# Optimization experiments

Hardware: AMD Instinct MI355X
Metric: run time of the kernel (lower is better)

The kernel has to match this reference:

```python
import jax, jax.numpy as jnp
import numpy as np

N_NODES = 50000
N_EDGES = 600000
D = 128
HIDDEN = 128
N_GRAPHS = 128
N_CLASSES = 10
N_STACKED = 3  # num_layers - 1


def setup_inputs() -> dict:
    key = jax.random.key(0)
    ks = jax.random.split(key, 12)
    s = 1.0 / np.sqrt(HIDDEN)
    inp = {
        "x": jax.random.normal(ks[0], (N_NODES, D), dtype=jnp.float32),
        "edge_index": jax.random.randint(ks[1], (2, N_EDGES), 0, N_NODES, dtype=jnp.int64),
        "batch": jnp.sort(jax.random.randint(ks[2], (N_NODES,), 0, N_GRAPHS, dtype=jnp.int64)),
        "W1": jax.random.normal(ks[3], (D, HIDDEN), dtype=jnp.float32) * s,
        "R1": jax.random.normal(ks[4], (D, HIDDEN), dtype=jnp.float32) * s,
        "b1": jnp.zeros((HIDDEN,), dtype=jnp.float32),
        "Wc": jax.random.normal(ks[5], (N_STACKED, HIDDEN, HIDDEN), dtype=jnp.float32) * s,
        "Rc": jax.random.normal(ks[6], (N_STACKED, HIDDEN, HIDDEN), dtype=jnp.float32) * s,
        "bc": jnp.zeros((N_STACKED, HIDDEN), dtype=jnp.float32),
        "lin1_w": jax.random.normal(ks[7], (HIDDEN, HIDDEN), dtype=jnp.float32) * s,
        "lin1_b": jnp.zeros((HIDDEN,), dtype=jnp.float32),
        "lin2_w": jax.random.normal(ks[8], (HIDDEN, N_CLASSES), dtype=jnp.float32) * s,
        "lin2_b": jnp.zeros((N_CLASSES,), dtype=jnp.float32),
    }
    return inp


def _gcn_norm(edge_index, n_nodes):
    # symmetric GCN normalization coeffs per edge (edge_weight=None -> ones)
    src, dst = edge_index[0], edge_index[1]
    ones = jnp.ones((edge_index.shape[1],), dtype=jnp.float32)
    deg = jax.ops.segment_sum(ones, dst, num_segments=n_nodes)
    dinv = jnp.where(deg > 0, jax.lax.rsqrt(jnp.maximum(deg, 1.0)), 0.0)
    return dinv[src] * dinv[dst]


def _gcs(x, src, dst, norm, W, R, b):
    # GCN aggregation on transformed features + linear skip (root) connection
    h = x @ W                                   # [N, H]
    msg = h[src] * norm[:, None]                # gather + scale, [E, H]
    agg = jax.ops.segment_sum(msg, dst, num_segments=x.shape[0])
    return agg + x @ R + b


def reference(x, edge_index, batch, W1, R1, b1, Wc, Rc, bc,
              lin1_w, lin1_b, lin2_w, lin2_b):
    src, dst = edge_index[0], edge_index[1]
    norm = _gcn_norm(edge_index, x.shape[0])

    h = jax.nn.relu(_gcs(x, src, dst, norm, W1, R1, b1))
    for i in range(N_STACKED):
        h = jax.nn.relu(_gcs(h, src, dst, norm, Wc[i], Rc[i], bc[i]))
    last = h

    # global mean pool over graphs
    sums = jax.ops.segment_sum(h, batch, num_segments=N_GRAPHS)
    cnts = jax.ops.segment_sum(jnp.ones((h.shape[0],), h.dtype), batch,
                               num_segments=N_GRAPHS)
    pooled = sums / jnp.maximum(cnts, 1.0)[:, None]

    g = jax.nn.relu(pooled @ lin1_w + lin1_b)   # dropout is identity in eval mode
    logits = g @ lin2_w + lin2_b
    return jax.nn.log_softmax(logits, axis=-1), last
```

## Files before the change

### kernel.cpp

```cpp
#include <hip/hip_runtime.h>

#define N_NODES  50000
#define N_EDGES  600000
#define DIM      128
#define N_GRAPHS 128
#define N_CLASSES 10
#define NB_SCAN  196
#define LDSW     136
#define NZB      6266


typedef __bf16 bf16x8 __attribute__((ext_vector_type(8)));
typedef float  f32x4  __attribute__((ext_vector_type(4)));

__device__ inline unsigned short f2bf(float f) {
  union { float f; unsigned int i; } u; u.f = f;
  unsigned int r = u.i + 0x7fff + ((u.i >> 16) & 1);
  return (unsigned short)(r >> 16);
}
__device__ inline float bf2f(unsigned short s) {
  union { unsigned int i; float f; } u; u.i = ((unsigned int)s) << 16;
  return u.f;
}
__device__ inline bf16x8 pack8(float4 lo, float4 hi) {
  union { bf16x8 v; unsigned short s[8]; } u;
  u.s[0] = f2bf(lo.x); u.s[1] = f2bf(lo.y); u.s[2] = f2bf(lo.z); u.s[3] = f2bf(lo.w);
  u.s[4] = f2bf(hi.x); u.s[5] = f2bf(hi.y); u.s[6] = f2bf(hi.z); u.s[7] = f2bf(hi.w);
  return u.v;
}


__global__ __launch_bounds__(256) void k_prep(float* __restrict__ zbase,
                                              const float* __restrict__ W1,
                                              const float* __restrict__ R1,
                                              const float* __restrict__ Wc,
                                              const float* __restrict__ Rc,
                                              unsigned short* __restrict__ pk) {
  if (blockIdx.x < NZB) {
    int i = blockIdx.x * 256 + threadIdx.x;
    if (i < 1604000) zbase[i] = 0.f;
    return;
  }
  int pb = blockIdx.x - NZB;
  int mm = pb >> 3, sub = pb & 7;
  const float* src = (mm == 0) ? W1
                   : (mm < 4)  ? Wc + (size_t)(mm - 1) * DIM * DIM
                   : (mm == 4) ? R1
                               : Rc + (size_t)(mm - 5) * DIM * DIM;
  int idx = sub * 256 + threadIdx.x;
  int lane = idx & 63;
  int kc   = (idx >> 6) & 3;
  int nt   = idx >> 8;
  int col  = nt * 16 + (lane & 15);
  int k0   = kc * 32 + (lane >> 4) * 8;
  unsigned short* dst = pk + (size_t)mm * 16384 + (size_t)idx * 8;
  ushort4 u;
  u.x = f2bf(src[(k0 + 0) * DIM + col]);
  u.y = f2bf(src[(k0 + 1) * DIM + col]);
  u.z = f2bf(src[(k0 + 2) * DIM + col]);
  u.w = f2bf(src[(k0 + 3) * DIM + col]);
  *(ushort4*)&dst[0] = u;
  u.x = f2bf(src[(k0 + 4) * DIM + col]);
  u.y = f2bf(src[(k0 + 5) * DIM + col]);
  u.z = f2bf(src[(k0 + 6) * DIM + col]);
  u.w = f2bf(src[(k0 + 7) * DIM + col]);
  *(ushort4*)&dst[4] = u;
}


__global__ __launch_bounds__(256) void k_deg(const int* __restrict__ ei,
                                             int* __restrict__ deg) {
  int e = blockIdx.x * 256 + threadIdx.x;
  if (e < N_EDGES) atomicAdd(&deg[ei[N_EDGES + e]], 1);
}

__global__ __launch_bounds__(256) void k_dinvsum(const int* __restrict__ deg,
                                                 float* __restrict__ dinv,
                                                 int* __restrict__ bsum) {
  int i = blockIdx.x * 256 + threadIdx.x;
  int t = threadIdx.x;
  int d = (i < N_NODES) ? deg[i] : 0;
  if (i < N_NODES) dinv[i] = (d > 0) ? rsqrtf((float)d) : 0.f;
  int dp = (d + 3) & ~3;
  __shared__ int tmp[256];
  tmp[t] = dp;
  __syncthreads();
  for (int off = 128; off > 0; off >>= 1) {
    if (t < off) tmp[t] += tmp[t + off];
    __syncthreads();
  }
  if (t == 0) bsum[blockIdx.x] = tmp[0];
}

__global__ __launch_bounds__(256) void k_bscan(const int* __restrict__ bsum,
                                               int* __restrict__ boff,
                                               int* __restrict__ rowp) {
  int t = threadIdx.x;
  int v = (t < NB_SCAN) ? bsum[t] : 0;
  __shared__ int tmp[256];
  tmp[t] = v;
  __syncthreads();
  for (int off = 1; off < 256; off <<= 1) {
    int add = (t >= off) ? tmp[t - off] : 0;
    __syncthreads();
    tmp[t] += add;
    __syncthreads();
  }
  boff[t] = tmp[t] - v;
  if (t == 255) rowp[N_NODES] = tmp[255];
}

__global__ __launch_bounds__(256) void k_rowp(const int* __restrict__ deg,
                                              const int* __restrict__ boff,
                                              int* __restrict__ rowp) {
  int i = blockIdx.x * 256 + threadIdx.x;
  int t = threadIdx.x;
  int dp = (i < N_NODES) ? ((deg[i] + 3) & ~3) : 0;
  __shared__ int tmp[256];
  tmp[t] = dp;
  __syncthreads();
  for (int off = 1; off < 256; off <<= 1) {
    int add = (t >= off) ? tmp[t - off] : 0;
    __syncthreads();
    tmp[t] += add;
    __syncthreads();
  }
  if (i < N_NODES) rowp[i] = boff[blockIdx.x] + tmp[t] - dp;
}

__global__ __launch_bounds__(256) void k_fill(const int* __restrict__ ei,
                                              const int* __restrict__ rowp,
                                              int* __restrict__ cnt,
                                              const float* __restrict__ dinv,
                                              int* __restrict__ csrc,
                                              float* __restrict__ enorm) {
  int e = blockIdx.x * 256 + threadIdx.x;
  if (e < N_EDGES) {
    int s = ei[e];
    int d = ei[N_EDGES + e];
    int p = rowp[d] + atomicAdd(&cnt[d], 1);
    csrc[p] = s;
    enorm[p] = dinv[s] * dinv[d];
  }
}


__global__ __launch_bounds__(256) void k_gemm0(const float* __restrict__ xf,
                                               const unsigned short* __restrict__ pkW,
                                               const unsigned short* __restrict__ pkR,
                                               const float* __restrict__ bv,
                                               unsigned short* __restrict__ hwb,
                                               unsigned short* __restrict__ skipb) {
  const int tid  = threadIdx.x;
  const int wave = tid >> 6, lane = tid & 63;
  const int m = lane & 15, q = lane >> 4;
  const int rbase = blockIdx.x * 64 + wave * 16;
  const int arow  = rbase + m;
  const bool aok  = arow < N_NODES;

  bf16x8 a[4];
#pragma unroll
  for (int kc = 0; kc < 4; ++kc) {
    float4 lo = make_float4(0.f, 0.f, 0.f, 0.f);
    float4 hi = make_float4(0.f, 0.f, 0.f, 0.f);
    if (aok) {
      lo = *(const float4*)&xf[arow * DIM + kc * 32 + q * 8];
      hi = *(const float4*)&xf[arow * DIM + kc * 32 + q * 8 + 4];
    }
    a[kc] = pack8(lo, hi);
  }

  f32x4 acc[16];
#pragma unroll
  for (int t = 0; t < 16; ++t) acc[t] = (f32x4){0.f, 0.f, 0.f, 0.f};

#pragma unroll
  for (int nt = 0; nt < 8; ++nt) {
    const unsigned short* pw = pkW + ((size_t)(nt * 4) * 64 + lane) * 8;
    const unsigned short* pr = pkR + ((size_t)(nt * 4) * 64 + lane) * 8;
#pragma unroll
    for (int kc = 0; kc < 4; ++kc) {
      bf16x8 bW = *(const bf16x8*)(pw + (size_t)kc * 64 * 8);
      acc[nt] = __builtin_amdgcn_mfma_f32_16x16x32_bf16(a[kc], bW, acc[nt], 0, 0, 0);
    }
#pragma unroll
    for (int kc = 0; kc < 4; ++kc) {
      bf16x8 bR = *(const bf16x8*)(pr + (size_t)kc * 64 * 8);
      acc[8 + nt] = __builtin_amdgcn_mfma_f32_16x16x32_bf16(a[kc], bR, acc[8 + nt], 0, 0, 0);
    }
  }

#pragma unroll
  for (int nt = 0; nt < 8; ++nt) {
    int col = nt * 16 + m;
    float bias = bv[col];
#pragma unroll
    for (int rg = 0; rg < 4; ++rg) {
      int row = rbase + q * 4 + rg;
      if (row < N_NODES) {
        hwb[row * DIM + col]   = f2bf(acc[nt][rg]);
        skipb[row * DIM + col] = f2bf(acc[8 + nt][rg] + bias);
      }
    }
  }
}


template<bool LAST>
__global__ __launch_bounds__(256) void k_aggemm(const unsigned short* __restrict__ hin,
                                                const int* __restrict__ rowp,
                                                const int* __restrict__ csrc,
                                                const float* __restrict__ enorm,
                                                const unsigned short* __restrict__ pkW,
                                                const unsigned short* __restrict__ pkR,
                                                const float* __restrict__ bv,
                                                unsigned short* __restrict__ hout,
                                                unsigned short* __restrict__ skipb,
                                                float* __restrict__ skipf) {
  __shared__ unsigned short xs[64 * LDSW];
  const int tid = threadIdx.x;
  const int row0 = blockIdx.x * 64;

  {
    int hw = tid >> 5;
    int l4 = (tid & 31) * 4;
    for (int rnd = 0; rnd < 8; ++rnd) {
      int n = row0 + rnd * 8 + hw;
      float4 acc = make_float4(0.f, 0.f, 0.f, 0.f);
      if (n < N_NODES) {
        ushort4 s = *(const ushort4*)&skipb[n * DIM + l4];
        acc = make_float4(bf2f(s.x), bf2f(s.y), bf2f(s.z), bf2f(s.w));
        int e0 = rowp[n], e1 = rowp[n + 1];
        for (int e = e0; e < e1; e += 4) {
          int4   cs = *(const int4*)&csrc[e];
          float4 wv = *(const float4*)&enorm[e];
          ushort4 u0 = *(const ushort4*)&hin[cs.x * DIM + l4];
          ushort4 u1 = *(const ushort4*)&hin[cs.y * DIM + l4];
          ushort4 u2 = *(const ushort4*)&hin[cs.z * DIM + l4];
          ushort4 u3 = *(const ushort4*)&hin[cs.w * DIM + l4];
          acc.x = fmaf(wv.x, bf2f(u0.x), fmaf(wv.y, bf2f(u1.x), fmaf(wv.z, bf2f(u2.x), fmaf(wv.w, bf2f(u3.x), acc.x))));
          acc.y = fmaf(wv.x, bf2f(u0.y), fmaf(wv.y, bf2f(u1.y), fmaf(wv.z, bf2f(u2.y), fmaf(wv.w, bf2f(u3.y), acc.y))));
          acc.z = fmaf(wv.x, bf2f(u0.z), fmaf(wv.y, bf2f(u1.z), fmaf(wv.z, bf2f(u2.z), fmaf(wv.w, bf2f(u3.z), acc.z))));
          acc.w = fmaf(wv.x, bf2f(u0.w), fmaf(wv.y, bf2f(u1.w), fmaf(wv.z, bf2f(u2.w), fmaf(wv.w, bf2f(u3.w), acc.w))));
        }
        acc.x = fmaxf(acc.x, 0.f);
        acc.y = fmaxf(acc.y, 0.f);
        acc.z = fmaxf(acc.z, 0.f);
        acc.w = fmaxf(acc.w, 0.f);
      }
      int r = rnd * 8 + hw;
      ushort4 o;
      o.x = f2bf(acc.x); o.y = f2bf(acc.y); o.z = f2bf(acc.z); o.w = f2bf(acc.w);
      *(ushort4*)&xs[r * LDSW + l4] = o;
    }
  }
  __syncthreads();

  const int wave = tid >> 6, lane = tid & 63;
  const int m = lane & 15, q = lane >> 4;
  const int rbase = row0 + wave * 16;

  bf16x8 a[4];
#pragma unroll
  for (int kc = 0; kc < 4; ++kc)
    a[kc] = *(const bf16x8*)&xs[(wave * 16 + m) * LDSW + kc * 32 + q * 8];

  f32x4 acc[16];
#pragma unroll
  for (int t = 0; t < 16; ++t) acc[t] = (f32x4){0.f, 0.f, 0.f, 0.f};

#pragma unroll
  for (int nt = 0; nt < 8; ++nt) {
    const unsigned short* pw = pkW + ((size_t)(nt * 4) * 64 + lane) * 8;
    const unsigned short* pr = pkR + ((size_t)(nt * 4) * 64 + lane) * 8;
#pragma unroll
    for (int kc = 0; kc < 4; ++kc) {
      bf16x8 bW = *(const bf16x8*)(pw + (size_t)kc * 64 * 8);
      acc[nt] = __builtin_amdgcn_mfma_f32_16x16x32_bf16(a[kc], bW, acc[nt], 0, 0, 0);
    }
#pragma unroll
    for (int kc = 0; kc < 4; ++kc) {
      bf16x8 bR = *(const bf16x8*)(pr + (size_t)kc * 64 * 8);
      acc[8 + nt] = __builtin_amdgcn_mfma_f32_16x16x32_bf16(a[kc], bR, acc[8 + nt], 0, 0, 0);
    }
  }

#pragma unroll
  for (int nt = 0; nt < 8; ++nt) {
    int col = nt * 16 + m;
    float bias = bv[col];
#pragma unroll
    for (int rg = 0; rg < 4; ++rg) {
      int row = rbase + q * 4 + rg;
      if (row < N_NODES) {
        hout[row * DIM + col] = f2bf(acc[nt][rg]);
        float v = acc[8 + nt][rg] + bias;
        if (LAST) skipf[row * DIM + col] = v;
        else      skipb[row * DIM + col] = f2bf(v);
      }
    }
  }
}


__global__ __launch_bounds__(256) void k_aggF(const unsigned short* __restrict__ hwb,
                                              const int* __restrict__ rowp,
                                              const int* __restrict__ csrc,
                                              const float* __restrict__ enorm,
                                              float* __restrict__ actf) {
  int n = blockIdx.x * 8 + (threadIdx.x >> 5);
  if (n >= N_NODES) return;
  int l4 = (threadIdx.x & 31) * 4;
  float4 acc = *(const float4*)&actf[n * DIM + l4];
  int e0 = rowp[n], e1 = rowp[n + 1];
  for (int e = e0; e < e1; e += 4) {
    int4   cs = *(const int4*)&csrc[e];
    float4 wv = *(const float4*)&enorm[e];
    ushort4 u0 = *(const ushort4*)&hwb[cs.x * DIM + l4];
    ushort4 u1 = *(const ushort4*)&hwb[cs.y * DIM + l4];
    ushort4 u2 = *(const ushort4*)&hwb[cs.z * DIM + l4];
    ushort4 u3 = *(const ushort4*)&hwb[cs.w * DIM + l4];
    acc.x = fmaf(wv.x, bf2f(u0.x), fmaf(wv.y, bf2f(u1.x), fmaf(wv.z, bf2f(u2.x), fmaf(wv.w, bf2f(u3.x), acc.x))));
    acc.y = fmaf(wv.x, bf2f(u0.y), fmaf(wv.y, bf2f(u1.y), fmaf(wv.z, bf2f(u2.y), fmaf(wv.w, bf2f(u3.y), acc.y))));
    acc.z = fmaf(wv.x, bf2f(u0.z), fmaf(wv.y, bf2f(u1.z), fmaf(wv.z, bf2f(u2.z), fmaf(wv.w, bf2f(u3.z), acc.z))));
    acc.w = fmaf(wv.x, bf2f(u0.w), fmaf(wv.y, bf2f(u1.w), fmaf(wv.z, bf2f(u2.w), fmaf(wv.w, bf2f(u3.w), acc.w))));
  }
  acc.x = fmaxf(acc.x, 0.f);
  acc.y = fmaxf(acc.y, 0.f);
  acc.z = fmaxf(acc.z, 0.f);
  acc.w = fmaxf(acc.w, 0.f);
  *(float4*)&actf[n * DIM + l4] = acc;
}


__global__ __launch_bounds__(1024) void k_pool2(const float* __restrict__ h,
                                                const int* __restrict__ batch,
                                                float* __restrict__ pooled) {
  int g = blockIdx.x;
  int t = threadIdx.x;
  __shared__ int sb[2];
  if (t < 2) {
    int target = g + t;
    int lo = 0, hi = N_NODES;
    while (lo < hi) {
      int mid = (lo + hi) >> 1;
      if (batch[mid] < target) lo = mid + 1; else hi = mid;
    }
    sb[t] = lo;
  }
  __syncthreads();
  int start = sb[0], end = sb[1];
  int c = t & 127, rg = t >> 7;
  float acc = 0.f;
  for (int r = start + rg; r < end; r += 8) acc += h[r * DIM + c];
  __shared__ float sp[8][DIM];
  sp[rg][c] = acc;
  __syncthreads();
  if (rg == 0) {
    float tot = acc;
#pragma unroll
    for (int i = 1; i < 8; ++i) tot += sp[i][c];
    float cnt = fmaxf((float)(end - start), 1.f);
    pooled[g * DIM + c] = tot / cnt;
  }
}


__global__ __launch_bounds__(128) void k_mlp1(const float* __restrict__ pooled,
                                              const float* __restrict__ w,
                                              const float* __restrict__ bias,
                                              float* __restrict__ g1) {
  int g = blockIdx.x, t = threadIdx.x;
  __shared__ float sp[DIM];
  sp[t] = pooled[g * DIM + t];
  __syncthreads();
  float acc = bias[t];
#pragma unroll 4
  for (int k = 0; k < DIM; ++k) acc = fmaf(sp[k], w[k * DIM + t], acc);
  g1[g * DIM + t] = fmaxf(acc, 0.f);
}

__global__ __launch_bounds__(128) void k_mlp2(const float* __restrict__ g1,
                                              const float* __restrict__ w,
                                              const float* __restrict__ bias,
                                              float* __restrict__ out) {
  int g = threadIdx.x;
  float l[N_CLASSES];
#pragma unroll
  for (int c = 0; c < N_CLASSES; ++c) l[c] = bias[c];
  for (int k = 0; k < DIM; ++k) {
    float gv = g1[g * DIM + k];
#pragma unroll
    for (int c = 0; c < N_CLASSES; ++c) l[c] = fmaf(gv, w[k * N_CLASSES + c], l[c]);
  }
  float m = l[0];
#pragma unroll
  for (int c = 1; c < N_CLASSES; ++c) m = fmaxf(m, l[c]);
  float s = 0.f;
#pragma unroll
  for (int c = 0; c < N_CLASSES; ++c) s += expf(l[c] - m);
  float lse = logf(s) + m;
#pragma unroll
  for (int c = 0; c < N_CLASSES; ++c) out[g * N_CLASSES + c] = l[c] - lse;
}


extern "C" void kernel_launch(void* const* d_in, const int* in_sizes, int n_in,
                              void* d_out, int out_size, void* d_ws, size_t ws_size,
                              hipStream_t stream) {
  const float* x     = (const float*)d_in[0];
  const int* ei      = (const int*)d_in[1];
  const int* batch   = (const int*)d_in[2];
  const float* W1  = (const float*)d_in[3];
  const float* R1  = (const float*)d_in[4];
  const float* b1  = (const float*)d_in[5];
  const float* Wc  = (const float*)d_in[6];
  const float* Rc  = (const float*)d_in[7];
  const float* bc  = (const float*)d_in[8];
  const float* l1w = (const float*)d_in[9];
  const float* l1b = (const float*)d_in[10];
  const float* l2w = (const float*)d_in[11];
  const float* l2b = (const float*)d_in[12];

  float* out   = (float*)d_out;
  float* dlast = out + N_GRAPHS * N_CLASSES;

  float* ws = (float*)d_ws;
  unsigned short* h0    = (unsigned short*)ws;
  unsigned short* h1    = (unsigned short*)(ws + 3200000);
  unsigned short* skipb = (unsigned short*)(ws + 6400000);
  int*   deg   = (int*)(ws + 9600000);
  int*   cnt   = (int*)(ws + 9650000);
  int*   csrc  = (int*)(ws + 9700000);
  float* enorm = ws + 10452000;
  float* dinv  = ws + 11204000;
  int*   rowp  = (int*)(ws + 11254000);
  float* pooled= ws + 11304016;
  float* g1    = ws + 11320400;
  unsigned short* pk = (unsigned short*)(ws + 11336784);
  int*   bsum  = (int*)(ws + 11402320);
  int*   boff  = (int*)(ws + 11402576);

  k_prep<<<NZB + 64, 256, 0, stream>>>(ws + 9600000, W1, R1, Wc, Rc, pk);
  k_deg <<<(N_EDGES + 255) / 256, 256, 0, stream>>>(ei, deg);
  k_dinvsum<<<NB_SCAN, 256, 0, stream>>>(deg, dinv, bsum);
  k_bscan<<<1, 256, 0, stream>>>(bsum, boff, rowp);
  k_rowp<<<NB_SCAN, 256, 0, stream>>>(deg, boff, rowp);
  k_fill<<<(N_EDGES + 255) / 256, 256, 0, stream>>>(ei, rowp, cnt, dinv, csrc, enorm);

  const int NGB = (N_NODES + 63) / 64;
  const int NAB = (N_NODES + 7) / 8;

  k_gemm0<<<NGB, 256, 0, stream>>>(x, pk + 0 * 16384, pk + 4 * 16384, b1, h0, skipb);
  k_aggemm<false><<<NGB, 256, 0, stream>>>(h0, rowp, csrc, enorm,
      pk + 1 * 16384, pk + 5 * 16384, bc + 0 * DIM, h1, skipb, nullptr);
  k_aggemm<false><<<NGB, 256, 0, stream>>>(h1, rowp, csrc, enorm,
      pk + 2 * 16384, pk + 6 * 16384, bc + 1 * DIM, h0, skipb, nullptr);
  k_aggemm<true><<<NGB, 256, 0, stream>>>(h0, rowp, csrc, enorm,
      pk + 3 * 16384, pk + 7 * 16384, bc + 2 * DIM, h1, skipb, dlast);
  k_aggF<<<NAB, 256, 0, stream>>>(h1, rowp, csrc, enorm, dlast);

  k_pool2<<<N_GRAPHS, 1024, 0, stream>>>(dlast, batch, pooled);
  k_mlp1<<<N_GRAPHS, 128, 0, stream>>>(pooled, l1w, l1b, g1);
  k_mlp2<<<1, N_GRAPHS, 0, stream>>>(g1, l2w, l2b, out);
}
```

Baseline: 394.4 us.

## Quantize gathered node features to int8 with per-row scales and pack edge data

The transformed features that are gathered per edge are now stored as int8 with a per-row absmax scale instead of bf16, which halves the bytes read in the gather-heavy aggregation kernels. Edge source index and normalization weight are interleaved into one int2 array, so each edge group needs one contiguous load stream instead of two. The zeroing in the prep kernel now uses float4 stores. The cost is an extra row-max reduction and quantization in the GEMM epilogues and a per-edge scale lookup, plus lower numerical precision that may fail the tolerance check.

```diff
diff --git a/kernel.cpp b/kernel.cpp
--- a/kernel.cpp
+++ b/kernel.cpp
@@ -7,7 +7,8 @@
 #define N_CLASSES 10
 #define NB_SCAN  196
 #define LDSW     136
-#define NZB      6266
+#define ZWORDS   1600032
+#define NZB4     1563
 
 
 typedef __bf16 bf16x8 __attribute__((ext_vector_type(8)));
@@ -28,20 +29,24 @@
   u.s[4] = f2bf(hi.x); u.s[5] = f2bf(hi.y); u.s[6] = f2bf(hi.z); u.s[7] = f2bf(hi.w);
   return u.v;
 }
-
-
-__global__ __launch_bounds__(256) void k_prep(float* __restrict__ zbase,
+__device__ inline float b2f0(unsigned u){ return (float)((int)(u<<24)>>24); }
+__device__ inline float b2f1(unsigned u){ return (float)((int)(u<<16)>>24); }
+__device__ inline float b2f2(unsigned u){ return (float)((int)(u<< 8)>>24); }
+__device__ inline float b2f3(unsigned u){ return (float)((int) u     >>24); }
+
+
+__global__ __launch_bounds__(256) void k_prep(float4* __restrict__ z4,
                                               const float* __restrict__ W1,
                                               const float* __restrict__ R1,
                                               const float* __restrict__ Wc,
                                               const float* __restrict__ Rc,
                                               unsigned short* __restrict__ pk) {
-  if (blockIdx.x < NZB) {
+  if (blockIdx.x < NZB4) {
     int i = blockIdx.x * 256 + threadIdx.x;
-    if (i < 1604000) zbase[i] = 0.f;
+    if (i < ZWORDS / 4) z4[i] = make_float4(0.f, 0.f, 0.f, 0.f);
     return;
   }
-  int pb = blockIdx.x - NZB;
+  int pb = blockIdx.x - NZB4;
   int mm = pb >> 3, sub = pb & 7;
   const float* src = (mm == 0) ? W1
                    : (mm < 4)  ? Wc + (size_t)(mm - 1) * DIM * DIM
@@ -132,15 +137,13 @@
                                               const int* __restrict__ rowp,
                                               int* __restrict__ cnt,
                                               const float* __restrict__ dinv,
-                                              int* __restrict__ csrc,
-                                              float* __restrict__ enorm) {
+                                              int2* __restrict__ epk) {
   int e = blockIdx.x * 256 + threadIdx.x;
   if (e < N_EDGES) {
     int s = ei[e];
     int d = ei[N_EDGES + e];
     int p = rowp[d] + atomicAdd(&cnt[d], 1);
-    csrc[p] = s;
-    enorm[p] = dinv[s] * dinv[d];
+    epk[p] = make_int2(s, __float_as_int(dinv[s] * dinv[d]));
   }
 }
 
@@ -149,7 +152,8 @@
                                                const unsigned short* __restrict__ pkW,
                                                const unsigned short* __restrict__ pkR,
                                                const float* __restrict__ bv,
-                                               unsigned short* __restrict__ hwb,
+                                               signed char* __restrict__ hq,
+                                               float* __restrict__ hsc,
                                                unsigned short* __restrict__ skipb) {
   const int tid  = threadIdx.x;
   const int wave = tid >> 6, lane = tid & 63;
@@ -190,6 +194,39 @@
     }
   }
 
+  float am[4], inv[4];
+#pragma unroll
+  for (int rg = 0; rg < 4; ++rg) {
+    float v = 0.f;
+#pragma unroll
+    for (int nt = 0; nt < 8; ++nt) v = fmaxf(v, fabsf(acc[nt][rg]));
+    am[rg] = v;
+  }
+#pragma unroll
+  for (int mask = 1; mask <= 8; mask <<= 1) {
+#pragma unroll
+    for (int rg = 0; rg < 4; ++rg)
+      am[rg] = fmaxf(am[rg], __shfl_xor(am[rg], mask, 64));
+  }
+#pragma unroll
+  for (int rg = 0; rg < 4; ++rg) inv[rg] = (am[rg] > 0.f) ? 127.f / am[rg] : 0.f;
+  if (m == 0) {
+#pragma unroll
+    for (int rg = 0; rg < 4; ++rg) {
+      int row = rbase + q * 4 + rg;
+      if (row < N_NODES) hsc[row] = am[rg] * (1.f / 127.f);
+    }
+  }
+#pragma unroll
+  for (int nt = 0; nt < 8; ++nt) {
+    int col = nt * 16 + m;
+#pragma unroll
+    for (int rg = 0; rg < 4; ++rg) {
+      int row = rbase + q * 4 + rg;
+      if (row < N_NODES)
+        hq[row * DIM + col] = (signed char)__float2int_rn(acc[nt][rg] * inv[rg]);
+    }
+  }
 #pragma unroll
   for (int nt = 0; nt < 8; ++nt) {
     int col = nt * 16 + m;
@@ -197,24 +234,22 @@
 #pragma unroll
     for (int rg = 0; rg < 4; ++rg) {
       int row = rbase + q * 4 + rg;
-      if (row < N_NODES) {
-        hwb[row * DIM + col]   = f2bf(acc[nt][rg]);
-        skipb[row * DIM + col] = f2bf(acc[8 + nt][rg] + bias);
-      }
+      if (row < N_NODES) skipb[row * DIM + col] = f2bf(acc[8 + nt][rg] + bias);
     }
   }
 }
 
 
 template<bool LAST>
-__global__ __launch_bounds__(256) void k_aggemm(const unsigned short* __restrict__ hin,
+__global__ __launch_bounds__(256) void k_aggemm(const signed char* __restrict__ hq,
+                                                const float* __restrict__ hsc,
                                                 const int* __restrict__ rowp,
-                                                const int* __restrict__ csrc,
-                                                const float* __restrict__ enorm,
+                                                const int2* __restrict__ epk,
                                                 const unsigned short* __restrict__ pkW,
                                                 const unsigned short* __restrict__ pkR,
                                                 const float* __restrict__ bv,
-                                                unsigned short* __restrict__ hout,
+                                                signed char* __restrict__ hoq,
+                                                float* __restrict__ hosc,
                                                 unsigned short* __restrict__ skipb,
                                                 float* __restrict__ skipf) {
   __shared__ unsigned short xs[64 * LDSW];
@@ -232,16 +267,20 @@
         acc = make_float4(bf2f(s.x), bf2f(s.y), bf2f(s.z), bf2f(s.w));
         int e0 = rowp[n], e1 = rowp[n + 1];
         for (int e = e0; e < e1; e += 4) {
-          int4   cs = *(const int4*)&csrc[e];
-          float4 wv = *(const float4*)&enorm[e];
-          ushort4 u0 = *(const ushort4*)&hin[cs.x * DIM + l4];
-          ushort4 u1 = *(const ushort4*)&hin[cs.y * DIM + l4];
-          ushort4 u2 = *(const ushort4*)&hin[cs.z * DIM + l4];
-          ushort4 u3 = *(const ushort4*)&hin[cs.w * DIM + l4];
-          acc.x = fmaf(wv.x, bf2f(u0.x), fmaf(wv.y, bf2f(u1.x), fmaf(wv.z, bf2f(u2.x), fmaf(wv.w, bf2f(u3.x), acc.x))));
-          acc.y = fmaf(wv.x, bf2f(u0.y), fmaf(wv.y, bf2f(u1.y), fmaf(wv.z, bf2f(u2.y), fmaf(wv.w, bf2f(u3.y), acc.y))));
-          acc.z = fmaf(wv.x, bf2f(u0.z), fmaf(wv.y, bf2f(u1.z), fmaf(wv.z, bf2f(u2.z), fmaf(wv.w, bf2f(u3.z), acc.z))));
-          acc.w = fmaf(wv.x, bf2f(u0.w), fmaf(wv.y, bf2f(u1.w), fmaf(wv.z, bf2f(u2.w), fmaf(wv.w, bf2f(u3.w), acc.w))));
+          int4 p0 = *(const int4*)&epk[e];
+          int4 p1 = *(const int4*)&epk[e + 2];
+          unsigned g0 = *(const unsigned*)&hq[p0.x * DIM + l4];
+          unsigned g1 = *(const unsigned*)&hq[p0.z * DIM + l4];
+          unsigned g2 = *(const unsigned*)&hq[p1.x * DIM + l4];
+          unsigned g3 = *(const unsigned*)&hq[p1.z * DIM + l4];
+          float w0 = __int_as_float(p0.y) * hsc[p0.x];
+          float w1 = __int_as_float(p0.w) * hsc[p0.z];
+          float w2 = __int_as_float(p1.y) * hsc[p1.x];
+          float w3 = __int_as_float(p1.w) * hsc[p1.z];
+          acc.x = fmaf(w0, b2f0(g0), fmaf(w1, b2f0(g1), fmaf(w2, b2f0(g2), fmaf(w3, b2f0(g3), acc.x))));
+          acc.y = fmaf(w0, b2f1(g0), fmaf(w1, b2f1(g1), fmaf(w2, b2f1(g2), fmaf(w3, b2f1(g3), acc.y))));
+          acc.z = fmaf(w0, b2f2(g0), fmaf(w1, b2f2(g1), fmaf(w2, b2f2(g2), fmaf(w3, b2f2(g3), acc.z))));
+          acc.w = fmaf(w0, b2f3(g0), fmaf(w1, b2f3(g1), fmaf(w2, b2f3(g2), fmaf(w3, b2f3(g3), acc.w))));
         }
         acc.x = fmaxf(acc.x, 0.f);
         acc.y = fmaxf(acc.y, 0.f);
@@ -285,6 +324,39 @@
     }
   }
 
+  float am[4], inv[4];
+#pragma unroll
+  for (int rg = 0; rg < 4; ++rg) {
+    float v = 0.f;
+#pragma unroll
+    for (int nt = 0; nt < 8; ++nt) v = fmaxf(v, fabsf(acc[nt][rg]));
+    am[rg] = v;
+  }
+#pragma unroll
+  for (int mask = 1; mask <= 8; mask <<= 1) {
+#pragma unroll
+    for (int rg = 0; rg < 4; ++rg)
+      am[rg] = fmaxf(am[rg], __shfl_xor(am[rg], mask, 64));
+  }
+#pragma unroll
+  for (int rg = 0; rg < 4; ++rg) inv[rg] = (am[rg] > 0.f) ? 127.f / am[rg] : 0.f;
+  if (m == 0) {
+#pragma unroll
+    for (int rg = 0; rg < 4; ++rg) {
+      int row = rbase + q * 4 + rg;
+      if (row < N_NODES) hosc[row] = am[rg] * (1.f / 127.f);
+    }
+  }
+#pragma unroll
+  for (int nt = 0; nt < 8; ++nt) {
+    int col = nt * 16 + m;
+#pragma unroll
+    for (int rg = 0; rg < 4; ++rg) {
+      int row = rbase + q * 4 + rg;
+      if (row < N_NODES)
+        hoq[row * DIM + col] = (signed char)__float2int_rn(acc[nt][rg] * inv[rg]);
+    }
+  }
 #pragma unroll
   for (int nt = 0; nt < 8; ++nt) {
     int col = nt * 16 + m;
@@ -293,7 +365,6 @@
     for (int rg = 0; rg < 4; ++rg) {
       int row = rbase + q * 4 + rg;
       if (row < N_NODES) {
-        hout[row * DIM + col] = f2bf(acc[nt][rg]);
         float v = acc[8 + nt][rg] + bias;
         if (LAST) skipf[row * DIM + col] = v;
         else      skipb[row * DIM + col] = f2bf(v);
@@ -303,10 +374,10 @@
 }
 
 
-__global__ __launch_bounds__(256) void k_aggF(const unsigned short* __restrict__ hwb,
+__global__ __launch_bounds__(256) void k_aggF(const signed char* __restrict__ hq,
+                                              const float* __restrict__ hsc,
                                               const int* __restrict__ rowp,
-                                              const int* __restrict__ csrc,
-                                              const float* __restrict__ enorm,
+                                              const int2* __restrict__ epk,
                                               float* __restrict__ actf) {
   int n = blockIdx.x * 8 + (threadIdx.x >> 5);
   if (n >= N_NODES) return;
@@ -314,16 +385,20 @@
   float4 acc = *(const float4*)&actf[n * DIM + l4];
   int e0 = rowp[n], e1 = rowp[n + 1];
   for (int e = e0; e < e1; e += 4) {
-    int4   cs = *(const int4*)&csrc[e];
-    float4 wv = *(const float4*)&enorm[e];
-    ushort4 u0 = *(const ushort4*)&hwb[cs.x * DIM + l4];
-    ushort4 u1 = *(const ushort4*)&hwb[cs.y * DIM + l4];
-    ushort4 u2 = *(const ushort4*)&hwb[cs.z * DIM + l4];
-    ushort4 u3 = *(const ushort4*)&hwb[cs.w * DIM + l4];
-    acc.x = fmaf(wv.x, bf2f(u0.x), fmaf(wv.y, bf2f(u1.x), fmaf(wv.z, bf2f(u2.x), fmaf(wv.w, bf2f(u3.x), acc.x))));
-    acc.y = fmaf(wv.x, bf2f(u0.y), fmaf(wv.y, bf2f(u1.y), fmaf(wv.z, bf2f(u2.y), fmaf(wv.w, bf2f(u3.y), acc.y))));
-    acc.z = fmaf(wv.x, bf2f(u0.z), fmaf(wv.y, bf2f(u1.z), fmaf(wv.z, bf2f(u2.z), fmaf(wv.w, bf2f(u3.z), acc.z))));
-    acc.w = fmaf(wv.x, bf2f(u0.w), fmaf(wv.y, bf2f(u1.w), fmaf(wv.z, bf2f(u2.w), fmaf(wv.w, bf2f(u3.w), acc.w))));
+    int4 p0 = *(const int4*)&epk[e];
+    int4 p1 = *(const int4*)&epk[e + 2];
+    unsigned g0 = *(const unsigned*)&hq[p0.x * DIM + l4];
+    unsigned g1 = *(const unsigned*)&hq[p0.z * DIM + l4];
+    unsigned g2 = *(const unsigned*)&hq[p1.x * DIM + l4];
+    unsigned g3 = *(const unsigned*)&hq[p1.z * DIM + l4];
+    float w0 = __int_as_float(p0.y) * hsc[p0.x];
+    float w1 = __int_as_float(p0.w) * hsc[p0.z];
+    float w2 = __int_as_float(p1.y) * hsc[p1.x];
+    float w3 = __int_as_float(p1.w) * hsc[p1.z];
+    acc.x = fmaf(w0, b2f0(g0), fmaf(w1, b2f0(g1), fmaf(w2, b2f0(g2), fmaf(w3, b2f0(g3), acc.x))));
+    acc.y = fmaf(w0, b2f1(g0), fmaf(w1, b2f1(g1), fmaf(w2, b2f1(g2), fmaf(w3, b2f1(g3), acc.y))));
+    acc.z = fmaf(w0, b2f2(g0), fmaf(w1, b2f2(g1), fmaf(w2, b2f2(g2), fmaf(w3, b2f2(g3), acc.z))));
+    acc.w = fmaf(w0, b2f3(g0), fmaf(w1, b2f3(g1), fmaf(w2, b2f3(g2), fmaf(w3, b2f3(g3), acc.w))));
   }
   acc.x = fmaxf(acc.x, 0.f);
   acc.y = fmaxf(acc.y, 0.f);
@@ -426,39 +501,41 @@
   float* dlast = out + N_GRAPHS * N_CLASSES;
 
   float* ws = (float*)d_ws;
-  unsigned short* h0    = (unsigned short*)ws;
-  unsigned short* h1    = (unsigned short*)(ws + 3200000);
-  unsigned short* skipb = (unsigned short*)(ws + 6400000);
-  int*   deg   = (int*)(ws + 9600000);
-  int*   cnt   = (int*)(ws + 9650000);
-  int*   csrc  = (int*)(ws + 9700000);
-  float* enorm = ws + 10452000;
-  float* dinv  = ws + 11204000;
-  int*   rowp  = (int*)(ws + 11254000);
-  float* pooled= ws + 11304016;
-  float* g1    = ws + 11320400;
-  unsigned short* pk = (unsigned short*)(ws + 11336784);
-  int*   bsum  = (int*)(ws + 11402320);
-  int*   boff  = (int*)(ws + 11402576);
-
-  k_prep<<<NZB + 64, 256, 0, stream>>>(ws + 9600000, W1, R1, Wc, Rc, pk);
+  signed char*    h0q   = (signed char*)ws;
+  signed char*    h1q   = (signed char*)(ws + 1601536);
+  unsigned short* skipb = (unsigned short*)(ws + 3203072);
+  int*   deg   = (int*)(ws + 6406144);
+  int*   cnt   = (int*)(ws + 6456144);
+  int2*  epk   = (int2*)(ws + 6506144);
+  float* dinv  = ws + 8006176;
+  int*   rowp  = (int*)(ws + 8056192);
+  float* h0sc  = ws + 8106208;
+  float* h1sc  = ws + 8156224;
+  float* pooled= ws + 8206240;
+  float* g1    = ws + 8222624;
+  unsigned short* pk = (unsigned short*)(ws + 8239008);
+  int*   bsum  = (int*)(ws + 8304544);
+  int*   boff  = (int*)(ws + 8304800);
+
+  k_prep<<<NZB4 + 64, 256, 0, stream>>>((float4*)(ws + 6406144), W1, R1, Wc, Rc, pk);
   k_deg <<<(N_EDGES + 255) / 256, 256, 0, stream>>>(ei, deg);
   k_dinvsum<<<NB_SCAN, 256, 0, stream>>>(deg, dinv, bsum);
   k_bscan<<<1, 256, 0, stream>>>(bsum, boff, rowp);
   k_rowp<<<NB_SCAN, 256, 0, stream>>>(deg, boff, rowp);
-  k_fill<<<(N_EDGES + 255) / 256, 256, 0, stream>>>(ei, rowp, cnt, dinv, csrc, enorm);
+  k_fill<<<(N_EDGES + 255) / 256, 256, 0, stream>>>(ei, rowp, cnt, dinv, epk);
 
   const int NGB = (N_NODES + 63) / 64;
   const int NAB = (N_NODES + 7) / 8;
 
-  k_gemm0<<<NGB, 256, 0, stream>>>(x, pk + 0 * 16384, pk + 4 * 16384, b1, h0, skipb);
-  k_aggemm<false><<<NGB, 256, 0, stream>>>(h0, rowp, csrc, enorm,
-      pk + 1 * 16384, pk + 5 * 16384, bc + 0 * DIM, h1, skipb, nullptr);
-  k_aggemm<false><<<NGB, 256, 0, stream>>>(h1, rowp, csrc, enorm,
-      pk + 2 * 16384, pk + 6 * 16384, bc + 1 * DIM, h0, skipb, nullptr);
-  k_aggemm<true><<<NGB, 256, 0, stream>>>(h0, rowp, csrc, enorm,
-      pk + 3 * 16384, pk + 7 * 16384, bc + 2 * DIM, h1, skipb, dlast);
-  k_aggF<<<NAB, 256, 0, stream>>>(h1, rowp, csrc, enorm, dlast);
+  k_gemm0<<<NGB, 256, 0, stream>>>(x, pk + 0 * 16384, pk + 4 * 16384, b1,
+                                   h0q, h0sc, skipb);
+  k_aggemm<false><<<NGB, 256, 0, stream>>>(h0q, h0sc, rowp, epk,
+      pk + 1 * 16384, pk + 5 * 16384, bc + 0 * DIM, h1q, h1sc, skipb, nullptr);
+  k_aggemm<false><<<NGB, 256, 0, stream>>>(h1q, h1sc, rowp, epk,
+      pk + 2 * 16384, pk + 6 * 16384, bc + 1 * DIM, h0q, h0sc, skipb, nullptr);
+  k_aggemm<true><<<NGB, 256, 0, stream>>>(h0q, h0sc, rowp, epk,
+      pk + 3 * 16384, pk + 7 * 16384, bc + 2 * DIM, h1q, h1sc, skipb, dlast);
+  k_aggF<<<NAB, 256, 0, stream>>>(h1q, h1sc, rowp, epk, dlast);
 
   k_pool2<<<N_GRAPHS, 1024, 0, stream>>>(dlast, batch, pooled);
   k_mlp1<<<N_GRAPHS, 128, 0, stream>>>(pooled, l1w, l1b, g1);
```

New measurement: 511.3 us. 1.3x slower.

## Interleave CSR source and norm, make aggregation rows wave-local, vectorize zeroing

Applied to the files above, without the earlier changes.

Packs each CSR edge's source index and normalization weight into one int2 array, so the gather loop fetches both with one 16-byte load per two edges instead of two separate streams. Remaps aggregation rows so each wave fills exactly the 16 LDS rows its own MFMA reads, which lets the block-wide barrier be dropped. The skip term is now loaded after the edge loop instead of before it, and the workspace zeroing uses float4 stores. Dropping the barrier depends on the wave-to-row mapping matching the later LDS reads exactly, and the workspace offsets were shifted for 16-byte alignment.

```diff
diff --git a/kernel.cpp b/kernel.cpp
--- a/kernel.cpp
+++ b/kernel.cpp
@@ -7,7 +7,8 @@
 #define N_CLASSES 10
 #define NB_SCAN  196
 #define LDSW     136
-#define NZB      6266
+#define ZWORDS   1700000
+#define NZB4     1661
 
 
 typedef __bf16 bf16x8 __attribute__((ext_vector_type(8)));
@@ -30,18 +31,18 @@
 }
 
 
-__global__ __launch_bounds__(256) void k_prep(float* __restrict__ zbase,
+__global__ __launch_bounds__(256) void k_prep(float4* __restrict__ z4,
                                               const float* __restrict__ W1,
                                               const float* __restrict__ R1,
                                               const float* __restrict__ Wc,
                                               const float* __restrict__ Rc,
                                               unsigned short* __restrict__ pk) {
-  if (blockIdx.x < NZB) {
+  if (blockIdx.x < NZB4) {
     int i = blockIdx.x * 256 + threadIdx.x;
-    if (i < 1604000) zbase[i] = 0.f;
+    if (i < ZWORDS / 4) z4[i] = make_float4(0.f, 0.f, 0.f, 0.f);
     return;
   }
-  int pb = blockIdx.x - NZB;
+  int pb = blockIdx.x - NZB4;
   int mm = pb >> 3, sub = pb & 7;
   const float* src = (mm == 0) ? W1
                    : (mm < 4)  ? Wc + (size_t)(mm - 1) * DIM * DIM
@@ -132,15 +133,13 @@
                                               const int* __restrict__ rowp,
                                               int* __restrict__ cnt,
                                               const float* __restrict__ dinv,
-                                              int* __restrict__ csrc,
-                                              float* __restrict__ enorm) {
+                                              int2* __restrict__ epk) {
   int e = blockIdx.x * 256 + threadIdx.x;
   if (e < N_EDGES) {
     int s = ei[e];
     int d = ei[N_EDGES + e];
     int p = rowp[d] + atomicAdd(&cnt[d], 1);
-    csrc[p] = s;
-    enorm[p] = dinv[s] * dinv[d];
+    epk[p] = make_int2(s, __float_as_int(dinv[s] * dinv[d]));
   }
 }
 
@@ -209,8 +208,7 @@
 template<bool LAST>
 __global__ __launch_bounds__(256) void k_aggemm(const unsigned short* __restrict__ hin,
                                                 const int* __restrict__ rowp,
-                                                const int* __restrict__ csrc,
-                                                const float* __restrict__ enorm,
+                                                const int2* __restrict__ epk,
                                                 const unsigned short* __restrict__ pkW,
                                                 const unsigned short* __restrict__ pkR,
                                                 const float* __restrict__ bv,
@@ -220,43 +218,43 @@
   __shared__ unsigned short xs[64 * LDSW];
   const int tid = threadIdx.x;
   const int row0 = blockIdx.x * 64;
+  const int wave = tid >> 6, lane = tid & 63;
 
   {
-    int hw = tid >> 5;
+    int h  = (tid >> 5) & 1;
     int l4 = (tid & 31) * 4;
     for (int rnd = 0; rnd < 8; ++rnd) {
-      int n = row0 + rnd * 8 + hw;
+      int r = wave * 16 + rnd * 2 + h;
+      int n = row0 + r;
       float4 acc = make_float4(0.f, 0.f, 0.f, 0.f);
       if (n < N_NODES) {
-        ushort4 s = *(const ushort4*)&skipb[n * DIM + l4];
-        acc = make_float4(bf2f(s.x), bf2f(s.y), bf2f(s.z), bf2f(s.w));
         int e0 = rowp[n], e1 = rowp[n + 1];
         for (int e = e0; e < e1; e += 4) {
-          int4   cs = *(const int4*)&csrc[e];
-          float4 wv = *(const float4*)&enorm[e];
-          ushort4 u0 = *(const ushort4*)&hin[cs.x * DIM + l4];
-          ushort4 u1 = *(const ushort4*)&hin[cs.y * DIM + l4];
-          ushort4 u2 = *(const ushort4*)&hin[cs.z * DIM + l4];
-          ushort4 u3 = *(const ushort4*)&hin[cs.w * DIM + l4];
-          acc.x = fmaf(wv.x, bf2f(u0.x), fmaf(wv.y, bf2f(u1.x), fmaf(wv.z, bf2f(u2.x), fmaf(wv.w, bf2f(u3.x), acc.x))));
-          acc.y = fmaf(wv.x, bf2f(u0.y), fmaf(wv.y, bf2f(u1.y), fmaf(wv.z, bf2f(u2.y), fmaf(wv.w, bf2f(u3.y), acc.y))));
-          acc.z = fmaf(wv.x, bf2f(u0.z), fmaf(wv.y, bf2f(u1.z), fmaf(wv.z, bf2f(u2.z), fmaf(wv.w, bf2f(u3.z), acc.z))));
-          acc.w = fmaf(wv.x, bf2f(u0.w), fmaf(wv.y, bf2f(u1.w), fmaf(wv.z, bf2f(u2.w), fmaf(wv.w, bf2f(u3.w), acc.w))));
+          int4 p0 = *(const int4*)&epk[e];
+          int4 p1 = *(const int4*)&epk[e + 2];
+          ushort4 u0 = *(const ushort4*)&hin[p0.x * DIM + l4];
+          ushort4 u1 = *(const ushort4*)&hin[p0.z * DIM + l4];
+          ushort4 u2 = *(const ushort4*)&hin[p1.x * DIM + l4];
+          ushort4 u3 = *(const ushort4*)&hin[p1.z * DIM + l4];
+          float w0 = __int_as_float(p0.y), w1 = __int_as_float(p0.w);
+          float w2 = __int_as_float(p1.y), w3 = __int_as_float(p1.w);
+          acc.x = fmaf(w0, bf2f(u0.x), fmaf(w1, bf2f(u1.x), fmaf(w2, bf2f(u2.x), fmaf(w3, bf2f(u3.x), acc.x))));
+          acc.y = fmaf(w0, bf2f(u0.y), fmaf(w1, bf2f(u1.y), fmaf(w2, bf2f(u2.y), fmaf(w3, bf2f(u3.y), acc.y))));
+          acc.z = fmaf(w0, bf2f(u0.z), fmaf(w1, bf2f(u1.z), fmaf(w2, bf2f(u2.z), fmaf(w3, bf2f(u3.z), acc.z))));
+          acc.w = fmaf(w0, bf2f(u0.w), fmaf(w1, bf2f(u1.w), fmaf(w2, bf2f(u2.w), fmaf(w3, bf2f(u3.w), acc.w))));
         }
-        acc.x = fmaxf(acc.x, 0.f);
-        acc.y = fmaxf(acc.y, 0.f);
-        acc.z = fmaxf(acc.z, 0.f);
-        acc.w = fmaxf(acc.w, 0.f);
+        ushort4 s = *(const ushort4*)&skipb[n * DIM + l4];
+        acc.x = fmaxf(acc.x + bf2f(s.x), 0.f);
+        acc.y = fmaxf(acc.y + bf2f(s.y), 0.f);
+        acc.z = fmaxf(acc.z + bf2f(s.z), 0.f);
+        acc.w = fmaxf(acc.w + bf2f(s.w), 0.f);
       }
-      int r = rnd * 8 + hw;
       ushort4 o;
       o.x = f2bf(acc.x); o.y = f2bf(acc.y); o.z = f2bf(acc.z); o.w = f2bf(acc.w);
       *(ushort4*)&xs[r * LDSW + l4] = o;
     }
   }
-  __syncthreads();
-
-  const int wave = tid >> 6, lane = tid & 63;
+
   const int m = lane & 15, q = lane >> 4;
   const int rbase = row0 + wave * 16;
 
@@ -305,30 +303,32 @@
 
 __global__ __launch_bounds__(256) void k_aggF(const unsigned short* __restrict__ hwb,
                                               const int* __restrict__ rowp,
-                                              const int* __restrict__ csrc,
-                                              const float* __restrict__ enorm,
+                                              const int2* __restrict__ epk,
                                               float* __restrict__ actf) {
   int n = blockIdx.x * 8 + (threadIdx.x >> 5);
   if (n >= N_NODES) return;
   int l4 = (threadIdx.x & 31) * 4;
-  float4 acc = *(const float4*)&actf[n * DIM + l4];
+  float4 acc = make_float4(0.f, 0.f, 0.f, 0.f);
   int e0 = rowp[n], e1 = rowp[n + 1];
   for (int e = e0; e < e1; e += 4) {
-    int4   cs = *(const int4*)&csrc[e];
-    float4 wv = *(const float4*)&enorm[e];
-    ushort4 u0 = *(const ushort4*)&hwb[cs.x * DIM + l4];
-    ushort4 u1 = *(const ushort4*)&hwb[cs.y * DIM + l4];
-    ushort4 u2 = *(const ushort4*)&hwb[cs.z * DIM + l4];
-    ushort4 u3 = *(const ushort4*)&hwb[cs.w * DIM + l4];
-    acc.x = fmaf(wv.x, bf2f(u0.x), fmaf(wv.y, bf2f(u1.x), fmaf(wv.z, bf2f(u2.x), fmaf(wv.w, bf2f(u3.x), acc.x))));
-    acc.y = fmaf(wv.x, bf2f(u0.y), fmaf(wv.y, bf2f(u1.y), fmaf(wv.z, bf2f(u2.y), fmaf(wv.w, bf2f(u3.y), acc.y))));
-    acc.z = fmaf(wv.x, bf2f(u0.z), fmaf(wv.y, bf2f(u1.z), fmaf(wv.z, bf2f(u2.z), fmaf(wv.w, bf2f(u3.z), acc.z))));
-    acc.w = fmaf(wv.x, bf2f(u0.w), fmaf(wv.y, bf2f(u1.w), fmaf(wv.z, bf2f(u2.w), fmaf(wv.w, bf2f(u3.w), acc.w))));
-  }
-  acc.x = fmaxf(acc.x, 0.f);
-  acc.y = fmaxf(acc.y, 0.f);
-  acc.z = fmaxf(acc.z, 0.f);
-  acc.w = fmaxf(acc.w, 0.f);
+    int4 p0 = *(const int4*)&epk[e];
+    int4 p1 = *(const int4*)&epk[e + 2];
+    ushort4 u0 = *(const ushort4*)&hwb[p0.x * DIM + l4];
+    ushort4 u1 = *(const ushort4*)&hwb[p0.z * DIM + l4];
+    ushort4 u2 = *(const ushort4*)&hwb[p1.x * DIM + l4];
+    ushort4 u3 = *(const ushort4*)&hwb[p1.z * DIM + l4];
+    float w0 = __int_as_float(p0.y), w1 = __int_as_float(p0.w);
+    float w2 = __int_as_float(p1.y), w3 = __int_as_float(p1.w);
+    acc.x = fmaf(w0, bf2f(u0.x), fmaf(w1, bf2f(u1.x), fmaf(w2, bf2f(u2.x), fmaf(w3, bf2f(u3.x), acc.x))));
+    acc.y = fmaf(w0, bf2f(u0.y), fmaf(w1, bf2f(u1.y), fmaf(w2, bf2f(u2.y), fmaf(w3, bf2f(u3.y), acc.y))));
+    acc.z = fmaf(w0, bf2f(u0.z), fmaf(w1, bf2f(u1.z), fmaf(w2, bf2f(u2.z), fmaf(w3, bf2f(u3.z), acc.z))));
+    acc.w = fmaf(w0, bf2f(u0.w), fmaf(w1, bf2f(u1.w), fmaf(w2, bf2f(u2.w), fmaf(w3, bf2f(u3.w), acc.w))));
+  }
+  float4 s = *(const float4*)&actf[n * DIM + l4];
+  acc.x = fmaxf(acc.x + s.x, 0.f);
+  acc.y = fmaxf(acc.y + s.y, 0.f);
+  acc.z = fmaxf(acc.z + s.z, 0.f);
+  acc.w = fmaxf(acc.w + s.w, 0.f);
   *(float4*)&actf[n * DIM + l4] = acc;
 }
 
@@ -427,38 +427,37 @@
 
   float* ws = (float*)d_ws;
   unsigned short* h0    = (unsigned short*)ws;
-  unsigned short* h1    = (unsigned short*)(ws + 3200000);
-  unsigned short* skipb = (unsigned short*)(ws + 6400000);
-  int*   deg   = (int*)(ws + 9600000);
-  int*   cnt   = (int*)(ws + 9650000);
-  int*   csrc  = (int*)(ws + 9700000);
-  float* enorm = ws + 10452000;
-  float* dinv  = ws + 11204000;
-  int*   rowp  = (int*)(ws + 11254000);
-  float* pooled= ws + 11304016;
-  float* g1    = ws + 11320400;
-  unsigned short* pk = (unsigned short*)(ws + 11336784);
-  int*   bsum  = (int*)(ws + 11402320);
-  int*   boff  = (int*)(ws + 11402576);
-
-  k_prep<<<NZB + 64, 256, 0, stream>>>(ws + 9600000, W1, R1, Wc, Rc, pk);
+  unsigned short* h1    = (unsigned short*)(ws + 3203072);
+  unsigned short* skipb = (unsigned short*)(ws + 6406144);
+  int*   deg   = (int*)(ws + 9609216);
+  int*   cnt   = (int*)(ws + 9659216);
+  int2*  epk   = (int2*)(ws + 9709216);
+  float* dinv  = ws + 11309216;
+  int*   rowp  = (int*)(ws + 11359216);
+  float* pooled= ws + 11409232;
+  float* g1    = ws + 11425616;
+  unsigned short* pk = (unsigned short*)(ws + 11442000);
+  int*   bsum  = (int*)(ws + 11507536);
+  int*   boff  = (int*)(ws + 11507792);
+
+  k_prep<<<NZB4 + 64, 256, 0, stream>>>((float4*)(ws + 9609216), W1, R1, Wc, Rc, pk);
   k_deg <<<(N_EDGES + 255) / 256, 256, 0, stream>>>(ei, deg);
   k_dinvsum<<<NB_SCAN, 256, 0, stream>>>(deg, dinv, bsum);
   k_bscan<<<1, 256, 0, stream>>>(bsum, boff, rowp);
   k_rowp<<<NB_SCAN, 256, 0, stream>>>(deg, boff, rowp);
-  k_fill<<<(N_EDGES + 255) / 256, 256, 0, stream>>>(ei, rowp, cnt, dinv, csrc, enorm);
+  k_fill<<<(N_EDGES + 255) / 256, 256, 0, stream>>>(ei, rowp, cnt, dinv, epk);
 
   const int NGB = (N_NODES + 63) / 64;
   const int NAB = (N_NODES + 7) / 8;
 
   k_gemm0<<<NGB, 256, 0, stream>>>(x, pk + 0 * 16384, pk + 4 * 16384, b1, h0, skipb);
-  k_aggemm<false><<<NGB, 256, 0, stream>>>(h0, rowp, csrc, enorm,
+  k_aggemm<false><<<NGB, 256, 0, stream>>>(h0, rowp, epk,
       pk + 1 * 16384, pk + 5 * 16384, bc + 0 * DIM, h1, skipb, nullptr);
-  k_aggemm<false><<<NGB, 256, 0, stream>>>(h1, rowp, csrc, enorm,
+  k_aggemm<false><<<NGB, 256, 0, stream>>>(h1, rowp, epk,
       pk + 2 * 16384, pk + 6 * 16384, bc + 1 * DIM, h0, skipb, nullptr);
-  k_aggemm<true><<<NGB, 256, 0, stream>>>(h0, rowp, csrc, enorm,
+  k_aggemm<true><<<NGB, 256, 0, stream>>>(h0, rowp, epk,
       pk + 3 * 16384, pk + 7 * 16384, bc + 2 * DIM, h1, skipb, dlast);
-  k_aggF<<<NAB, 256, 0, stream>>>(h1, rowp, csrc, enorm, dlast);
+  k_aggF<<<NAB, 256, 0, stream>>>(h1, rowp, epk, dlast);
 
   k_pool2<<<N_GRAPHS, 1024, 0, stream>>>(dlast, batch, pooled);
   k_mlp1<<<N_GRAPHS, 128, 0, stream>>>(pooled, l1w, l1b, g1);
```

Result: no change. 394.2 us (-0.1%).
